# Kernel optimization log

Hardware: AMD Instinct MI355X
Metric: run time of the kernel (lower is better)

## Reference

```python
import jax, jax.numpy as jnp
import numpy as np
import math

PAD = 1
V = 30527
D = 768
H = 12
HD = D // H
FF = 3072
L = 6
B = 1
S = 2048
WIN = 128
NB = 32          # relative_attention_num_buckets
MAXD = 128       # max_distance in relative_position_bucket
POS = S + PAD + 1  # learned positional table size (fairseq offset convention)


def _rel_bucket(rp):
    # Faithful port of FlexSentenceEncoder.relative_position_bucket (bidirectional)
    n = -rp
    nb = NB // 2
    ret = (n < 0).astype(jnp.int32) * nb
    n = jnp.abs(n)
    max_exact = nb // 2
    is_small = n < max_exact
    val_large = max_exact + (
        jnp.log(jnp.maximum(n, 1).astype(jnp.float32) / max_exact)
        / math.log(MAXD / max_exact) * (nb - max_exact)
    ).astype(jnp.int32)
    val_large = jnp.minimum(val_large, nb - 1)
    return ret + jnp.where(is_small, n, val_large)


def _ln(x, s, b):
    m = jnp.mean(x, axis=-1, keepdims=True)
    v = jnp.mean((x - m) ** 2, axis=-1, keepdims=True)
    return (x - m) / jnp.sqrt(v + 1e-5) * s + b


def setup_inputs() -> dict:
    key = jax.random.key(0)
    ks = jax.random.split(key, 16)
    def nrm(k, shape, scale=0.02):
        return jax.random.normal(k, shape, jnp.float32) * scale
    tokens = jax.random.randint(ks[0], (B, S), 0, V)
    segment_labels = jax.random.randint(ks[1], (B, S), 0, 2)
    embed_tokens = nrm(ks[2], (V, D)).at[PAD].set(0.0)  # padding_idx row is zero
    pos_emb = nrm(ks[3], (POS, D))
    seg_emb = nrm(ks[4], (2, D))
    rel_bias = nrm(ks[5], (NB, H))
    return {
        'tokens': tokens,
        'segment_labels': segment_labels,
        'embed_tokens': embed_tokens,
        'pos_emb': pos_emb,
        'seg_emb': seg_emb,
        'rel_bias': rel_bias,
        'Wq': nrm(ks[6], (L, D, D)), 'bq': jnp.zeros((L, D), jnp.float32),
        'Wk': nrm(ks[7], (L, D, D)), 'bk': jnp.zeros((L, D), jnp.float32),
        'Wv': nrm(ks[8], (L, D, D)), 'bv': jnp.zeros((L, D), jnp.float32),
        'Wo': nrm(ks[9], (L, D, D)), 'bo': jnp.zeros((L, D), jnp.float32),
        'ln1_s': jnp.ones((L, D), jnp.float32), 'ln1_b': jnp.zeros((L, D), jnp.float32),
        'W1': nrm(ks[10], (L, D, FF)), 'b1': jnp.zeros((L, FF), jnp.float32),
        'W2': nrm(ks[11], (L, FF, D)), 'b2': jnp.zeros((L, D), jnp.float32),
        'ln2_s': jnp.ones((L, D), jnp.float32), 'ln2_b': jnp.zeros((L, D), jnp.float32),
    }


def _forward(tokens, segment_labels, embed_tokens, pos_emb, seg_emb, rel_bias,
             Wq, bq, Wk, bk, Wv, bv, Wo, bo, ln1_s, ln1_b, W1, b1, W2, b2, ln2_s, ln2_b):
    pad = (tokens == PAD)                                # [B,S]
    nonpad = (~pad).astype(jnp.int32)
    x = embed_tokens[tokens]                             # [B,S,D]
    positions = PAD + jnp.cumsum(nonpad, axis=1) * nonpad  # fairseq make_positions
    x = x + pos_emb[positions] + seg_emb[segment_labels]
    x = x * (1.0 - pad[..., None].astype(x.dtype))

    idx = jnp.arange(S)
    rp = idx[None, :] - idx[:, None]                     # memory - context
    bias = rel_bias[_rel_bucket(rp)].transpose(2, 0, 1)  # [H,S,S]
    win_ok = jnp.abs(rp) <= WIN                          # sliding-window mask
    addmask = jnp.where(win_ok[None, None], 0.0, -1e30) \
        + jnp.where(pad, -1e30, 0.0)[:, None, None, :]   # [B,1,S,S]
    scale = 1.0 / math.sqrt(HD)

    def block(h, p):
        wq, bq_, wk, bk_, wv, bv_, wo, bo_, s1, sb1, w1, fb1, w2, fb2, s2, sb2 = p
        q = ((h @ wq + bq_) * scale).reshape(B, S, H, HD).transpose(0, 2, 1, 3)
        k = (h @ wk + bk_).reshape(B, S, H, HD).transpose(0, 2, 1, 3)
        v = (h @ wv + bv_).reshape(B, S, H, HD).transpose(0, 2, 1, 3)
        sc = jnp.einsum('bhqd,bhkd->bhqk', q, k) + bias[None] + addmask
        a = jax.nn.softmax(sc, axis=-1)
        o = jnp.einsum('bhqk,bhkd->bhqd', a, v).transpose(0, 2, 1, 3).reshape(B, S, D)
        o = o @ wo + bo_
        h = _ln(h + o, s1, sb1)                          # post-norm (normalize_before=False)
        f = jax.nn.relu(h @ w1 + fb1) @ w2 + fb2
        h = _ln(h + f, s2, sb2)
        return h, None

    params = (Wq, bq, Wk, bk, Wv, bv, Wo, bo, ln1_s, ln1_b, W1, b1, W2, b2, ln2_s, ln2_b)
    x, _ = jax.lax.scan(block, x, params)
    return x  # final hidden states [B,S,D]; sentence_rep = x[:,0,:]


def reference(tokens, segment_labels, embed_tokens, pos_emb, seg_emb, rel_bias,
              Wq, bq, Wk, bk, Wv, bv, Wo, bo, ln1_s, ln1_b, W1, b1, W2, b2, ln2_s, ln2_b):
    return _forward(tokens, segment_labels, embed_tokens, pos_emb, seg_emb, rel_bias,
                    Wq, bq, Wk, bk, Wv, bv, Wo, bo, ln1_s, ln1_b, W1, b1, W2, b2, ln2_s, ln2_b)
```

## Files before the change

kernel.cpp:

```cpp
#include <hip/hip_runtime.h>
#include <hip/hip_bf16.h>

#define S 2048
#define D 768
#define H 12
#define HD 64
#define FF 3072
#define NL 6
#define WIN 128
#define PADIDX 1

typedef __hip_bfloat16 bf16;
typedef __attribute__((ext_vector_type(8))) __bf16 bf16x8;
typedef __attribute__((ext_vector_type(4))) float f32x4;
typedef __attribute__((ext_vector_type(8))) unsigned short u16x8;

__device__ __forceinline__ unsigned short f2bfu(float f) {
    bf16 b = __float2bfloat16(f);
    return *(unsigned short*)&b;
}

__device__ __forceinline__ void g2l16(const bf16* g, bf16* l) {
    __builtin_amdgcn_global_load_lds((__attribute__((address_space(1))) void*)(g),
                                     (__attribute__((address_space(3))) void*)(l), 16, 0, 0);
}

__global__ void positions_kernel(const int* __restrict__ tokens, int* __restrict__ positions) {
    __shared__ int sums[256];
    int t = threadIdx.x;
    int np[8]; int loc = 0;
    for (int i = 0; i < 8; i++) { np[i] = (tokens[t * 8 + i] != PADIDX) ? 1 : 0; loc += np[i]; }
    sums[t] = loc;
    __syncthreads();
    for (int off = 1; off < 256; off <<= 1) {
        int u = (t >= off) ? sums[t - off] : 0;
        __syncthreads();
        sums[t] += u;
        __syncthreads();
    }
    int run = (t > 0) ? sums[t - 1] : 0;
    for (int i = 0; i < 8; i++) {
        run += np[i];
        positions[t * 8 + i] = np[i] ? (PADIDX + run) : PADIDX;
    }
}

__global__ void embed_kernel(const int* __restrict__ tokens, const int* __restrict__ seg,
                             const int* __restrict__ positions,
                             const float* __restrict__ emb, const float* __restrict__ pemb,
                             const float* __restrict__ semb,
                             float* __restrict__ h, bf16* __restrict__ h_bf) {
    int s = blockIdx.x, t = threadIdx.x;
    int tok = tokens[s];
    int pos = positions[s];
    int sg = seg[s];
    bool pad = (tok == PADIDX);
    for (int i = 0; i < 3; i++) {
        int c = t + i * 256;
        float val = emb[(size_t)tok * D + c] + pemb[(size_t)pos * D + c] + semb[(size_t)sg * D + c];
        if (pad) val = 0.0f;
        h[(size_t)s * D + c] = val;
        h_bf[(size_t)s * D + c] = __float2bfloat16(val);
    }
}

__global__ void transpose_convert(const float* __restrict__ src, bf16* __restrict__ dst,
                                  int K, int N, long srcLS, long dstLS) {
    src += (long)blockIdx.z * srcLS;
    dst += (long)blockIdx.z * dstLS;
    __shared__ float tile[64][65];
    int k0 = blockIdx.x * 64, n0 = blockIdx.y * 64;
    int t = threadIdx.x;
    for (int i = t; i < 4096; i += 256) {
        int r = i >> 6, c = i & 63;
        tile[r][c] = src[(long)(k0 + r) * N + n0 + c];
    }
    __syncthreads();
    for (int i = t; i < 4096; i += 256) {
        int r = i >> 6, c = i & 63;
        dst[(long)(n0 + r) * K + k0 + c] = __float2bfloat16(tile[c][r]);
    }
}

template <int MODE>
__global__ __launch_bounds__(256, 4) void gemm64(
    const bf16* __restrict__ A, const bf16* __restrict__ Bt,
    const float* __restrict__ bias0, const float* __restrict__ bias1, const float* __restrict__ bias2,
    float* __restrict__ outF, bf16* __restrict__ outB, int M, int N, int K, int klen) {
    __shared__ __align__(16) bf16 As[64 * 32];
    __shared__ __align__(16) bf16 Bs[128 * 32];
    int t = threadIdx.x;
    int lane = t & 63, w = t >> 6;
    int m0 = blockIdx.x * 64, n0 = blockIdx.y * 128;
    int kbase = blockIdx.z * klen;
    int wm = (w & 1) * 32, wn = (w >> 1) * 64;
    int qd = lane >> 4, l16 = lane & 15;

    f32x4 acc[2][4] = {};

    int i1 = t + 256;
    int oA  = ((t & 3) ^ ((t >> 3) & 3)) * 8;
    int oB1 = ((i1 & 3) ^ ((i1 >> 3) & 3)) * 8;
    const bf16* Ag  = A  + (size_t)(m0 + (t >> 2)) * K + kbase + oA;
    const bf16* Bg0 = Bt + (size_t)(n0 + (t >> 2)) * K + kbase + oA;
    const bf16* Bg1 = Bt + (size_t)(n0 + (i1 >> 2)) * K + kbase + oB1;
    bf16* Al  = As + (size_t)(t & ~63) * 8;
    bf16* Bl0 = Bs + (size_t)(t & ~63) * 8;
    bf16* Bl1 = Bs + (size_t)(256 + (t & ~63)) * 8;

    int soct = (qd ^ ((l16 >> 1) & 3)) * 8;

    int nkt = klen >> 5;
    for (int kt = 0; kt < nkt; ++kt) {
        int ko = kt * 32;
        g2l16(Ag + ko, Al);
        g2l16(Bg0 + ko, Bl0);
        g2l16(Bg1 + ko, Bl1);
        __syncthreads();
        bf16x8 aF[2], bF[4];
#pragma unroll
        for (int mi = 0; mi < 2; mi++) aF[mi] = *(const bf16x8*)&As[(wm + mi * 16 + l16) * 32 + soct];
#pragma unroll
        for (int ni = 0; ni < 4; ni++) bF[ni] = *(const bf16x8*)&Bs[(wn + ni * 16 + l16) * 32 + soct];
#pragma unroll
        for (int mi = 0; mi < 2; mi++)
#pragma unroll
            for (int ni = 0; ni < 4; ni++)
                acc[mi][ni] = __builtin_amdgcn_mfma_f32_16x16x32_bf16(aF[mi], bF[ni], acc[mi][ni], 0, 0, 0);
        __syncthreads();
    }

#pragma unroll
    for (int ni = 0; ni < 4; ni++) {
        int col = n0 + wn + ni * 16 + l16;
        float bb;
        if (MODE == 0) bb = (col < 768) ? bias0[col] : ((col < 1536) ? bias1[col - 768] : bias2[col - 1536]);
        else if (MODE == 1) bb = (blockIdx.z == 0) ? bias0[col] : 0.0f;
        else bb = bias0[col];
#pragma unroll
        for (int mi = 0; mi < 2; mi++) {
            int row = m0 + wm + mi * 16 + qd * 4;
#pragma unroll
            for (int r = 0; r < 4; r++) {
                float v = acc[mi][ni][r] + bb;
                if (MODE == 0) {
                    if (col < 768) v *= 0.125f;
                    outB[(size_t)(row + r) * N + col] = __float2bfloat16(v);
                } else if (MODE == 1) {
                    outF[(size_t)blockIdx.z * M * N + (size_t)(row + r) * N + col] = v;
                } else {
                    v = fmaxf(v, 0.0f);
                    outB[(size_t)(row + r) * N + col] = __float2bfloat16(v);
                }
            }
        }
    }
}

#define KT 288
#define KSTR 72
#define VSTR 296
__global__ __launch_bounds__(256, 2) void attn_kernel(const bf16* __restrict__ qkv,
                                                      const int* __restrict__ tokens,
                                                      const float* __restrict__ relb,
                                                      bf16* __restrict__ out) {
    const int q0 = blockIdx.x * 32;
    const int h = blockIdx.y;
    const int t = threadIdx.x;
    const int lane = t & 63, w = t >> 6;
    const int l16 = lane & 15, qd = lane >> 4;
    const int klo = max(0, q0 - WIN);

    __shared__ __align__(16) unsigned short KsPs[KT * KSTR];
    __shared__ __align__(16) unsigned short VtS[64 * VSTR];
    __shared__ float rbS[260];
    __shared__ float wmaxS[4][32];
    __shared__ float wsumS[4][32];
    __shared__ char kmS[KT];

    const unsigned short* qkvu = (const unsigned short*)qkv;

#pragma unroll
    for (int j = 0; j < 9; j++) {
        int i = j * 256 + t;
        int key = i >> 3, oct = i & 7;
        int ksrc = min(klo + key, S - 1);
        *(u16x8*)&KsPs[key * KSTR + oct * 8] =
            *(const u16x8*)(qkvu + (size_t)ksrc * 2304 + 768 + h * 64 + oct * 8);
    }
#pragma unroll
    for (int j = 0; j < 9; j++) {
        int i = j * 256 + t;
        int oct = i / KT;
        int key = i - oct * KT;
        int ksrc = min(klo + key, S - 1);
        u16x8 v = *(const u16x8*)(qkvu + (size_t)ksrc * 2304 + 1536 + h * 64 + oct * 8);
#pragma unroll
        for (int u = 0; u < 8; u++) VtS[(oct * 8 + u) * VSTR + key] = v[u];
    }
    for (int idx = t; idx < 260; idx += 256) {
        int dd = idx - 129;
        float bv = -1e30f;
        if (dd >= -128 && dd <= 128) {
            int ni = dd, ret = 0;
            if (ni < 0) { ret = 16; ni = -ni; }
            int val;
            if (ni < 8) val = ni;
            else {
                int m;
                if (ni < 12) m = 0; else if (ni < 16) m = 1; else if (ni < 23) m = 2;
                else if (ni < 32) m = 3; else if (ni < 46) m = 4; else if (ni < 64) m = 5;
                else if (ni < 91) m = 6; else if (ni < 128) m = 7; else m = 8;
                val = 8 + m;
                if (val > 15) val = 15;
            }
            bv = relb[(ret + val) * H + h];
        }
        rbS[idx] = bv;
    }
    for (int idx = t; idx < KT; idx += 256) {
        int key = klo + idx;
        kmS[idx] = (key < S && tokens[key] != PADIDX) ? 0 : 1;
    }
    __syncthreads();

    bf16x8 Qf[2][2];
#pragma unroll
    for (int qt = 0; qt < 2; qt++)
#pragma unroll
        for (int ko = 0; ko < 2; ko++)
            Qf[qt][ko] = *(const bf16x8*)(qkvu + (size_t)(q0 + qt * 16 + l16) * 2304 + h * 64 + ko * 32 + qd * 8);

    f32x4 acc[2][5] = {};
#pragma unroll
    for (int j = 0; j < 5; j++) {
        int kt = w + 4 * j;
        if (kt < 18) {
            bf16x8 b0 = *(const bf16x8*)&KsPs[(kt * 16 + l16) * KSTR + qd * 8];
            bf16x8 b1 = *(const bf16x8*)&KsPs[(kt * 16 + l16) * KSTR + 32 + qd * 8];
#pragma unroll
            for (int qt = 0; qt < 2; qt++) {
                acc[qt][j] = __builtin_amdgcn_mfma_f32_16x16x32_bf16(Qf[qt][0], b0, acc[qt][j], 0, 0, 0);
                acc[qt][j] = __builtin_amdgcn_mfma_f32_16x16x32_bf16(Qf[qt][1], b1, acc[qt][j], 0, 0, 0);
            }
        }
    }

    float rmax[2][4];
#pragma unroll
    for (int qt = 0; qt < 2; qt++)
#pragma unroll
        for (int r = 0; r < 4; r++) rmax[qt][r] = -3e38f;
    const int qmk = q0 - klo;
#pragma unroll
    for (int j = 0; j < 5; j++) {
        int kt = w + 4 * j;
        if (kt < 18) {
            int kidx = kt * 16 + l16;
            float km = kmS[kidx] ? -1e30f : 0.0f;
#pragma unroll
            for (int qt = 0; qt < 2; qt++)
#pragma unroll
                for (int r = 0; r < 4; r++) {
                    int dd = qmk + qt * 16 + qd * 4 + r - kidx;
                    dd = min(129, max(-129, dd));
                    float sc = acc[qt][j][r] + rbS[dd + 129] + km;
                    acc[qt][j][r] = sc;
                    rmax[qt][r] = fmaxf(rmax[qt][r], sc);
                }
        }
    }
#pragma unroll
    for (int m = 1; m < 16; m <<= 1)
#pragma unroll
        for (int qt = 0; qt < 2; qt++)
#pragma unroll
            for (int r = 0; r < 4; r++)
                rmax[qt][r] = fmaxf(rmax[qt][r], __shfl_xor(rmax[qt][r], m));
    if (l16 == 0) {
#pragma unroll
        for (int qt = 0; qt < 2; qt++)
#pragma unroll
            for (int r = 0; r < 4; r++) wmaxS[w][qt * 16 + qd * 4 + r] = rmax[qt][r];
    }
    __syncthreads();

    float gmax[2][4];
#pragma unroll
    for (int qt = 0; qt < 2; qt++)
#pragma unroll
        for (int r = 0; r < 4; r++) {
            int row = qt * 16 + qd * 4 + r;
            gmax[qt][r] = fmaxf(fmaxf(wmaxS[0][row], wmaxS[1][row]), fmaxf(wmaxS[2][row], wmaxS[3][row]));
        }

    float lsum[2][4] = {};
#pragma unroll
    for (int j = 0; j < 5; j++) {
        int kt = w + 4 * j;
        if (kt < 18) {
#pragma unroll
            for (int qt = 0; qt < 2; qt++)
#pragma unroll
                for (int r = 0; r < 4; r++) {
                    float p = __expf(acc[qt][j][r] - gmax[qt][r]);
                    lsum[qt][r] += p;
                    KsPs[(qt * 16 + qd * 4 + r) * VSTR + kt * 16 + l16] = f2bfu(p);
                }
        }
    }
#pragma unroll
    for (int m = 1; m < 16; m <<= 1)
#pragma unroll
        for (int qt = 0; qt < 2; qt++)
#pragma unroll
            for (int r = 0; r < 4; r++) lsum[qt][r] += __shfl_xor(lsum[qt][r], m);
    if (l16 == 0) {
#pragma unroll
        for (int qt = 0; qt < 2; qt++)
#pragma unroll
            for (int r = 0; r < 4; r++) wsumS[w][qt * 16 + qd * 4 + r] = lsum[qt][r];
    }
    __syncthreads();

    {
        int qt = w & 1, dt0 = (w >> 1) * 2;
        f32x4 o0 = {}, o1 = {};
#pragma unroll
        for (int kk = 0; kk < 9; kk++) {
            bf16x8 aP = *(const bf16x8*)&KsPs[(qt * 16 + l16) * VSTR + kk * 32 + qd * 8];
            bf16x8 v0 = *(const bf16x8*)&VtS[(dt0 * 16 + l16) * VSTR + kk * 32 + qd * 8];
            bf16x8 v1 = *(const bf16x8*)&VtS[((dt0 + 1) * 16 + l16) * VSTR + kk * 32 + qd * 8];
            o0 = __builtin_amdgcn_mfma_f32_16x16x32_bf16(aP, v0, o0, 0, 0, 0);
            o1 = __builtin_amdgcn_mfma_f32_16x16x32_bf16(aP, v1, o1, 0, 0, 0);
        }
#pragma unroll
        for (int r = 0; r < 4; r++) {
            int row = qt * 16 + qd * 4 + r;
            float ts = wsumS[0][row] + wsumS[1][row] + wsumS[2][row] + wsumS[3][row];
            float inv = 1.0f / ts;
            size_t obase = (size_t)(q0 + row) * D + h * 64;
            out[obase + dt0 * 16 + l16] = __float2bfloat16(o0[r] * inv);
            out[obase + (dt0 + 1) * 16 + l16] = __float2bfloat16(o1[r] * inv);
        }
    }
}

template <int NP>
__global__ __launch_bounds__(256) void ln_kernel(const float* __restrict__ x, const float* __restrict__ parts,
                                                 const float* __restrict__ sc, const float* __restrict__ bi,
                                                 float* __restrict__ out, bf16* __restrict__ out_bf) {
    int row = blockIdx.x, t = threadIdx.x;
    float v[3];
    float lsum = 0.0f, lsq = 0.0f;
#pragma unroll
    for (int i = 0; i < 3; i++) {
        int c = t + i * 256;
        size_t idx = (size_t)row * D + c;
        float val = x[idx];
#pragma unroll
        for (int p = 0; p < NP; p++) val += parts[(size_t)p * S * D + idx];
        v[i] = val; lsum += val; lsq += val * val;
    }
#pragma unroll
    for (int off = 32; off; off >>= 1) { lsum += __shfl_down(lsum, off); lsq += __shfl_down(lsq, off); }
    __shared__ float s1[4], s2[4];
    if ((t & 63) == 0) { s1[t >> 6] = lsum; s2[t >> 6] = lsq; }
    __syncthreads();
    float tot = s1[0] + s1[1] + s1[2] + s1[3];
    float tot2 = s2[0] + s2[1] + s2[2] + s2[3];
    float mean = tot * (1.0f / 768.0f);
    float var = tot2 * (1.0f / 768.0f) - mean * mean;
    float rstd = rsqrtf(var + 1e-5f);
#pragma unroll
    for (int i = 0; i < 3; i++) {
        int c = t + i * 256;
        float y = (v[i] - mean) * rstd * sc[c] + bi[c];
        out[(size_t)row * D + c] = y;
        out_bf[(size_t)row * D + c] = __float2bfloat16(y);
    }
}

extern "C" void kernel_launch(void* const* d_in, const int* in_sizes, int n_in,
                              void* d_out, int out_size, void* d_ws, size_t ws_size,
                              hipStream_t stream) {
    const int* tokens = (const int*)d_in[0];
    const int* seg = (const int*)d_in[1];
    const float* emb = (const float*)d_in[2];
    const float* pemb = (const float*)d_in[3];
    const float* semb = (const float*)d_in[4];
    const float* relb = (const float*)d_in[5];
    const float* Wq = (const float*)d_in[6];  const float* bq = (const float*)d_in[7];
    const float* Wk = (const float*)d_in[8];  const float* bk = (const float*)d_in[9];
    const float* Wv = (const float*)d_in[10]; const float* bv = (const float*)d_in[11];
    const float* Wo = (const float*)d_in[12]; const float* bo = (const float*)d_in[13];
    const float* ln1s = (const float*)d_in[14]; const float* ln1b = (const float*)d_in[15];
    const float* W1 = (const float*)d_in[16]; const float* b1 = (const float*)d_in[17];
    const float* W2 = (const float*)d_in[18]; const float* b2 = (const float*)d_in[19];
    const float* ln2s = (const float*)d_in[20]; const float* ln2b = (const float*)d_in[21];

    char* base = (char*)d_ws;
    size_t off = 0;
    auto take = [&](size_t bytes) -> char* {
        char* p = base + off;
        off = (off + bytes + 255) & ~(size_t)255;
        return p;
    };
    int* positions = (int*)take((size_t)S * 4);
    float* h       = (float*)take((size_t)S * D * 4);
    bf16* h_bf     = (bf16*)take((size_t)S * D * 2);
    float* parts   = (float*)take((size_t)4 * S * D * 4);
    bf16* qkv      = (bf16*)take((size_t)S * 2304 * 2);
    bf16* attnO    = (bf16*)take((size_t)S * D * 2);
    bf16* ff1      = (bf16*)take((size_t)S * FF * 2);
    bf16* Wqkv_t   = (bf16*)take((size_t)NL * 2304 * 768 * 2);
    bf16* Wo_t     = (bf16*)take((size_t)NL * 768 * 768 * 2);
    bf16* W1_t     = (bf16*)take((size_t)NL * 3072 * 768 * 2);
    bf16* W2_t     = (bf16*)take((size_t)NL * 768 * 3072 * 2);
    (void)ws_size; (void)n_in; (void)in_sizes;

    positions_kernel<<<1, 256, 0, stream>>>(tokens, positions);
    embed_kernel<<<S, 256, 0, stream>>>(tokens, seg, positions, emb, pemb, semb, h, h_bf);

    transpose_convert<<<dim3(12, 12, NL), 256, 0, stream>>>(Wq, Wqkv_t, 768, 768, 768L * 768, 2304L * 768);
    transpose_convert<<<dim3(12, 12, NL), 256, 0, stream>>>(Wk, Wqkv_t + 768L * 768, 768, 768, 768L * 768, 2304L * 768);
    transpose_convert<<<dim3(12, 12, NL), 256, 0, stream>>>(Wv, Wqkv_t + 1536L * 768, 768, 768, 768L * 768, 2304L * 768);
    transpose_convert<<<dim3(12, 12, NL), 256, 0, stream>>>(Wo, Wo_t, 768, 768, 768L * 768, 768L * 768);
    transpose_convert<<<dim3(12, 48, NL), 256, 0, stream>>>(W1, W1_t, 768, 3072, 768L * 3072, 3072L * 768);
    transpose_convert<<<dim3(48, 12, NL), 256, 0, stream>>>(W2, W2_t, 3072, 768, 3072L * 768, 768L * 3072);

    for (int l = 0; l < NL; l++) {
        gemm64<0><<<dim3(32, 18, 1), 256, 0, stream>>>(h_bf, Wqkv_t + (size_t)l * 2304 * 768,
                                                       bq + l * 768, bk + l * 768, bv + l * 768,
                                                       nullptr, qkv, S, 2304, 768, 768);
        attn_kernel<<<dim3(S / 32, H), 256, 0, stream>>>(qkv, tokens, relb, attnO);
        gemm64<1><<<dim3(32, 6, 2), 256, 0, stream>>>(attnO, Wo_t + (size_t)l * 768 * 768,
                                                      bo + l * 768, nullptr, nullptr,
                                                      parts, nullptr, S, 768, 768, 384);
        ln_kernel<2><<<S, 256, 0, stream>>>(h, parts, ln1s + l * 768, ln1b + l * 768, h, h_bf);
        gemm64<2><<<dim3(32, 24, 1), 256, 0, stream>>>(h_bf, W1_t + (size_t)l * 3072 * 768,
                                                       b1 + l * 3072, nullptr, nullptr,
                                                       nullptr, ff1, S, 3072, 768, 768);
        gemm64<1><<<dim3(32, 6, 4), 256, 0, stream>>>(ff1, W2_t + (size_t)l * 768 * 3072,
                                                      b2 + l * 768, nullptr, nullptr,
                                                      parts, nullptr, S, 768, 3072, 768);
        ln_kernel<4><<<S, 256, 0, stream>>>(h, parts, ln2s + l * 768, ln2b + l * 768, h, h_bf);
    }
    hipMemcpyAsync(d_out, h, (size_t)out_size * 4, hipMemcpyDeviceToDevice, stream);
}
```

Baseline: 965.0 us.

## Split attention keys into two chunks with online softmax to raise occupancy

The attention kernel now processes its key window in two chunks of 160 keys with an online-softmax rescale, instead of staging all 288 keys at once. This shrinks LDS per block so occupancy can go from 2 to 3 blocks per CU, and K is loaded with direct global-to-LDS loads into an XOR-swizzled layout to cut bank conflicts. The cost is extra barriers, a rescale step between chunks, and a second chunk that partly overlaps work the single-pass version did in one go.

```diff
diff --git a/kernel.cpp b/kernel.cpp
--- a/kernel.cpp
+++ b/kernel.cpp
@@ -157,10 +157,9 @@
     }
 }
 
-#define KT 288
-#define KSTR 72
-#define VSTR 296
-__global__ __launch_bounds__(256, 2) void attn_kernel(const bf16* __restrict__ qkv,
+#define KC 160
+#define VSTR2 168
+__global__ __launch_bounds__(256, 3) void attn_kernel(const bf16* __restrict__ qkv,
                                                       const int* __restrict__ tokens,
                                                       const float* __restrict__ relb,
                                                       bf16* __restrict__ out) {
@@ -170,34 +169,19 @@
     const int lane = t & 63, w = t >> 6;
     const int l16 = lane & 15, qd = lane >> 4;
     const int klo = max(0, q0 - WIN);
-
-    __shared__ __align__(16) unsigned short KsPs[KT * KSTR];
-    __shared__ __align__(16) unsigned short VtS[64 * VSTR];
+    const int khi = min(S - 1, q0 + 31 + WIN);
+    const int nk = khi - klo + 1;
+
+    __shared__ __align__(16) unsigned short KB[KC * 64];
+    __shared__ __align__(16) unsigned short VT[64 * VSTR2];
     __shared__ float rbS[260];
     __shared__ float wmaxS[4][32];
     __shared__ float wsumS[4][32];
-    __shared__ char kmS[KT];
+    __shared__ float mS[2][32];
+    __shared__ char kmS[320];
 
     const unsigned short* qkvu = (const unsigned short*)qkv;
 
-#pragma unroll
-    for (int j = 0; j < 9; j++) {
-        int i = j * 256 + t;
-        int key = i >> 3, oct = i & 7;
-        int ksrc = min(klo + key, S - 1);
-        *(u16x8*)&KsPs[key * KSTR + oct * 8] =
-            *(const u16x8*)(qkvu + (size_t)ksrc * 2304 + 768 + h * 64 + oct * 8);
-    }
-#pragma unroll
-    for (int j = 0; j < 9; j++) {
-        int i = j * 256 + t;
-        int oct = i / KT;
-        int key = i - oct * KT;
-        int ksrc = min(klo + key, S - 1);
-        u16x8 v = *(const u16x8*)(qkvu + (size_t)ksrc * 2304 + 1536 + h * 64 + oct * 8);
-#pragma unroll
-        for (int u = 0; u < 8; u++) VtS[(oct * 8 + u) * VSTR + key] = v[u];
-    }
     for (int idx = t; idx < 260; idx += 256) {
         int dd = idx - 129;
         float bv = -1e30f;
@@ -218,131 +202,184 @@
         }
         rbS[idx] = bv;
     }
-    for (int idx = t; idx < KT; idx += 256) {
+    for (int idx = t; idx < 320; idx += 256) {
         int key = klo + idx;
         kmS[idx] = (key < S && tokens[key] != PADIDX) ? 0 : 1;
     }
-    __syncthreads();
+    if (t < 32) mS[0][t] = -3e38f;
 
     bf16x8 Qf[2][2];
 #pragma unroll
-    for (int qt = 0; qt < 2; qt++)
+    for (int qt2 = 0; qt2 < 2; qt2++)
 #pragma unroll
         for (int ko = 0; ko < 2; ko++)
-            Qf[qt][ko] = *(const bf16x8*)(qkvu + (size_t)(q0 + qt * 16 + l16) * 2304 + h * 64 + ko * 32 + qd * 8);
-
-    f32x4 acc[2][5] = {};
-#pragma unroll
-    for (int j = 0; j < 5; j++) {
-        int kt = w + 4 * j;
-        if (kt < 18) {
-            bf16x8 b0 = *(const bf16x8*)&KsPs[(kt * 16 + l16) * KSTR + qd * 8];
-            bf16x8 b1 = *(const bf16x8*)&KsPs[(kt * 16 + l16) * KSTR + 32 + qd * 8];
-#pragma unroll
-            for (int qt = 0; qt < 2; qt++) {
-                acc[qt][j] = __builtin_amdgcn_mfma_f32_16x16x32_bf16(Qf[qt][0], b0, acc[qt][j], 0, 0, 0);
-                acc[qt][j] = __builtin_amdgcn_mfma_f32_16x16x32_bf16(Qf[qt][1], b1, acc[qt][j], 0, 0, 0);
-            }
-        }
-    }
-
-    float rmax[2][4];
-#pragma unroll
-    for (int qt = 0; qt < 2; qt++)
-#pragma unroll
-        for (int r = 0; r < 4; r++) rmax[qt][r] = -3e38f;
+            Qf[qt2][ko] = *(const bf16x8*)(qkvu + (size_t)(q0 + qt2 * 16 + l16) * 2304 + h * 64 + ko * 32 + qd * 8);
+
+    f32x4 o0 = {}, o1 = {};
+    float lrow[4] = {0.f, 0.f, 0.f, 0.f};
+    const int qt = w & 1, dt0 = (w >> 1) * 2;
     const int qmk = q0 - klo;
-#pragma unroll
-    for (int j = 0; j < 5; j++) {
-        int kt = w + 4 * j;
-        if (kt < 18) {
-            int kidx = kt * 16 + l16;
-            float km = kmS[kidx] ? -1e30f : 0.0f;
-#pragma unroll
-            for (int qt = 0; qt < 2; qt++)
-#pragma unroll
-                for (int r = 0; r < 4; r++) {
-                    int dd = qmk + qt * 16 + qd * 4 + r - kidx;
-                    dd = min(129, max(-129, dd));
-                    float sc = acc[qt][j][r] + rbS[dd + 129] + km;
-                    acc[qt][j][r] = sc;
-                    rmax[qt][r] = fmaxf(rmax[qt][r], sc);
+    const int rr8 = l16 & 7;
+
+    for (int c = 0; c < 2; ++c) {
+        const int kbase = c * KC;
+        const int kcnt = min(nk - kbase, KC);
+        if (kcnt <= 0) break;
+        if (c) __syncthreads();
+
+        {
+            const int rsub = lane >> 3;
+            const int o = (lane & 7) ^ rsub;
+            const int wr0 = w * 40;
+#pragma unroll
+            for (int j = 0; j < 5; ++j) {
+                int row = wr0 + j * 8 + rsub;
+                int ksrc = min(klo + kbase + row, S - 1);
+                g2l16((const bf16*)(qkvu + (size_t)ksrc * 2304 + 768 + h * 64 + o * 8),
+                      (bf16*)&KB[(wr0 + j * 8) * 64]);
+            }
+        }
+#pragma unroll
+        for (int jj = 0; jj < 5; ++jj) {
+            int i = jj * 256 + t;
+            int oct = i / KC;
+            int key = i - oct * KC;
+            int ksrc = min(klo + kbase + key, S - 1);
+            u16x8 v = *(const u16x8*)(qkvu + (size_t)ksrc * 2304 + 1536 + h * 64 + oct * 8);
+#pragma unroll
+            for (int u = 0; u < 8; ++u) VT[(oct * 8 + u) * VSTR2 + key] = v[u];
+        }
+        __syncthreads();
+
+        const int kt16 = kcnt >> 4;
+        f32x4 acc[2][3] = {};
+#pragma unroll
+        for (int j = 0; j < 3; ++j) {
+            int kt = w + 4 * j;
+            if (kt < kt16) {
+                const unsigned short* kr = &KB[(kt * 16 + l16) * 64];
+                bf16x8 b0 = *(const bf16x8*)&kr[(qd ^ rr8) * 8];
+                bf16x8 b1 = *(const bf16x8*)&kr[((4 | qd) ^ rr8) * 8];
+#pragma unroll
+                for (int q2 = 0; q2 < 2; ++q2) {
+                    acc[q2][j] = __builtin_amdgcn_mfma_f32_16x16x32_bf16(Qf[q2][0], b0, acc[q2][j], 0, 0, 0);
+                    acc[q2][j] = __builtin_amdgcn_mfma_f32_16x16x32_bf16(Qf[q2][1], b1, acc[q2][j], 0, 0, 0);
                 }
-        }
-    }
-#pragma unroll
-    for (int m = 1; m < 16; m <<= 1)
-#pragma unroll
-        for (int qt = 0; qt < 2; qt++)
-#pragma unroll
-            for (int r = 0; r < 4; r++)
-                rmax[qt][r] = fmaxf(rmax[qt][r], __shfl_xor(rmax[qt][r], m));
-    if (l16 == 0) {
-#pragma unroll
-        for (int qt = 0; qt < 2; qt++)
-#pragma unroll
-            for (int r = 0; r < 4; r++) wmaxS[w][qt * 16 + qd * 4 + r] = rmax[qt][r];
-    }
-    __syncthreads();
-
-    float gmax[2][4];
-#pragma unroll
-    for (int qt = 0; qt < 2; qt++)
-#pragma unroll
-        for (int r = 0; r < 4; r++) {
+            }
+        }
+
+        float rmax[2][4];
+#pragma unroll
+        for (int q2 = 0; q2 < 2; ++q2)
+#pragma unroll
+            for (int r = 0; r < 4; ++r) rmax[q2][r] = -3e38f;
+#pragma unroll
+        for (int j = 0; j < 3; ++j) {
+            int kt = w + 4 * j;
+            if (kt < kt16) {
+                int g = kbase + kt * 16 + l16;
+                float km = kmS[g] ? -1e30f : 0.0f;
+#pragma unroll
+                for (int q2 = 0; q2 < 2; ++q2)
+#pragma unroll
+                    for (int r = 0; r < 4; ++r) {
+                        int dd = qmk + q2 * 16 + qd * 4 + r - g;
+                        dd = min(129, max(-129, dd));
+                        float sc = acc[q2][j][r] + rbS[dd + 129] + km;
+                        acc[q2][j][r] = sc;
+                        rmax[q2][r] = fmaxf(rmax[q2][r], sc);
+                    }
+            }
+        }
+#pragma unroll
+        for (int m = 1; m < 16; m <<= 1)
+#pragma unroll
+            for (int q2 = 0; q2 < 2; ++q2)
+#pragma unroll
+                for (int r = 0; r < 4; ++r)
+                    rmax[q2][r] = fmaxf(rmax[q2][r], __shfl_xor(rmax[q2][r], m));
+        if (l16 == 0) {
+#pragma unroll
+            for (int q2 = 0; q2 < 2; ++q2)
+#pragma unroll
+                for (int r = 0; r < 4; ++r) wmaxS[w][q2 * 16 + qd * 4 + r] = rmax[q2][r];
+        }
+        __syncthreads();
+
+        float mnew[2][4], alpha[2][4];
+#pragma unroll
+        for (int q2 = 0; q2 < 2; ++q2)
+#pragma unroll
+            for (int r = 0; r < 4; ++r) {
+                int row = q2 * 16 + qd * 4 + r;
+                float cm = fmaxf(fmaxf(wmaxS[0][row], wmaxS[1][row]), fmaxf(wmaxS[2][row], wmaxS[3][row]));
+                float mp = mS[c & 1][row];
+                float mn = fmaxf(mp, cm);
+                mnew[q2][r] = mn;
+                alpha[q2][r] = __expf(mp - mn);
+            }
+        float ls[2][4] = {};
+#pragma unroll
+        for (int j = 0; j < 3; ++j) {
+            int kt = w + 4 * j;
+            if (kt < kt16) {
+#pragma unroll
+                for (int q2 = 0; q2 < 2; ++q2)
+#pragma unroll
+                    for (int r = 0; r < 4; ++r) {
+                        float p = __expf(acc[q2][j][r] - mnew[q2][r]);
+                        ls[q2][r] += p;
+                        KB[(q2 * 16 + qd * 4 + r) * VSTR2 + kt * 16 + l16] = f2bfu(p);
+                    }
+            }
+        }
+#pragma unroll
+        for (int m = 1; m < 16; m <<= 1)
+#pragma unroll
+            for (int q2 = 0; q2 < 2; ++q2)
+#pragma unroll
+                for (int r = 0; r < 4; ++r) ls[q2][r] += __shfl_xor(ls[q2][r], m);
+        if (l16 == 0) {
+#pragma unroll
+            for (int q2 = 0; q2 < 2; ++q2)
+#pragma unroll
+                for (int r = 0; r < 4; ++r) wsumS[w][q2 * 16 + qd * 4 + r] = ls[q2][r];
+        }
+        if (w == 0 && l16 == 0) {
+#pragma unroll
+            for (int q2 = 0; q2 < 2; ++q2)
+#pragma unroll
+                for (int r = 0; r < 4; ++r) mS[(c + 1) & 1][q2 * 16 + qd * 4 + r] = mnew[q2][r];
+        }
+        __syncthreads();
+
+        const int kk32 = kcnt >> 5;
+        f32x4 pv0 = {}, pv1 = {};
+        for (int kk = 0; kk < kk32; ++kk) {
+            bf16x8 aP = *(const bf16x8*)&KB[(qt * 16 + l16) * VSTR2 + kk * 32 + qd * 8];
+            bf16x8 v0 = *(const bf16x8*)&VT[(dt0 * 16 + l16) * VSTR2 + kk * 32 + qd * 8];
+            bf16x8 v1 = *(const bf16x8*)&VT[((dt0 + 1) * 16 + l16) * VSTR2 + kk * 32 + qd * 8];
+            pv0 = __builtin_amdgcn_mfma_f32_16x16x32_bf16(aP, v0, pv0, 0, 0, 0);
+            pv1 = __builtin_amdgcn_mfma_f32_16x16x32_bf16(aP, v1, pv1, 0, 0, 0);
+        }
+#pragma unroll
+        for (int r = 0; r < 4; ++r) {
             int row = qt * 16 + qd * 4 + r;
-            gmax[qt][r] = fmaxf(fmaxf(wmaxS[0][row], wmaxS[1][row]), fmaxf(wmaxS[2][row], wmaxS[3][row]));
-        }
-
-    float lsum[2][4] = {};
-#pragma unroll
-    for (int j = 0; j < 5; j++) {
-        int kt = w + 4 * j;
-        if (kt < 18) {
-#pragma unroll
-            for (int qt = 0; qt < 2; qt++)
-#pragma unroll
-                for (int r = 0; r < 4; r++) {
-                    float p = __expf(acc[qt][j][r] - gmax[qt][r]);
-                    lsum[qt][r] += p;
-                    KsPs[(qt * 16 + qd * 4 + r) * VSTR + kt * 16 + l16] = f2bfu(p);
-                }
-        }
-    }
-#pragma unroll
-    for (int m = 1; m < 16; m <<= 1)
-#pragma unroll
-        for (int qt = 0; qt < 2; qt++)
-#pragma unroll
-            for (int r = 0; r < 4; r++) lsum[qt][r] += __shfl_xor(lsum[qt][r], m);
-    if (l16 == 0) {
-#pragma unroll
-        for (int qt = 0; qt < 2; qt++)
-#pragma unroll
-            for (int r = 0; r < 4; r++) wsumS[w][qt * 16 + qd * 4 + r] = lsum[qt][r];
-    }
-    __syncthreads();
-
-    {
-        int qt = w & 1, dt0 = (w >> 1) * 2;
-        f32x4 o0 = {}, o1 = {};
-#pragma unroll
-        for (int kk = 0; kk < 9; kk++) {
-            bf16x8 aP = *(const bf16x8*)&KsPs[(qt * 16 + l16) * VSTR + kk * 32 + qd * 8];
-            bf16x8 v0 = *(const bf16x8*)&VtS[(dt0 * 16 + l16) * VSTR + kk * 32 + qd * 8];
-            bf16x8 v1 = *(const bf16x8*)&VtS[((dt0 + 1) * 16 + l16) * VSTR + kk * 32 + qd * 8];
-            o0 = __builtin_amdgcn_mfma_f32_16x16x32_bf16(aP, v0, o0, 0, 0, 0);
-            o1 = __builtin_amdgcn_mfma_f32_16x16x32_bf16(aP, v1, o1, 0, 0, 0);
-        }
-#pragma unroll
-        for (int r = 0; r < 4; r++) {
-            int row = qt * 16 + qd * 4 + r;
-            float ts = wsumS[0][row] + wsumS[1][row] + wsumS[2][row] + wsumS[3][row];
-            float inv = 1.0f / ts;
-            size_t obase = (size_t)(q0 + row) * D + h * 64;
-            out[obase + dt0 * 16 + l16] = __float2bfloat16(o0[r] * inv);
-            out[obase + (dt0 + 1) * 16 + l16] = __float2bfloat16(o1[r] * inv);
-        }
+            float a = alpha[qt][r];
+            float tot = wsumS[0][row] + wsumS[1][row] + wsumS[2][row] + wsumS[3][row];
+            lrow[r] = lrow[r] * a + tot;
+            o0[r] = o0[r] * a + pv0[r];
+            o1[r] = o1[r] * a + pv1[r];
+        }
+    }
+
+#pragma unroll
+    for (int r = 0; r < 4; ++r) {
+        int row = qt * 16 + qd * 4 + r;
+        float inv = 1.0f / lrow[r];
+        size_t ob = (size_t)(q0 + row) * D + h * 64;
+        out[ob + dt0 * 16 + l16] = __float2bfloat16(o0[r] * inv);
+        out[ob + (dt0 + 1) * 16 + l16] = __float2bfloat16(o1[r] * inv);
     }
 }
 
```

Result: no change. 970.4 us (+0.6%).
